# Performance work log

Hardware: AMD Instinct MI355X
Metric: run time of the kernel (lower is better)

The kernel has to match this reference:

```python
import jax, jax.numpy as jnp
import numpy as np

IN_FEATURES = 4096
OUT_FEATURES = 4096
IN_GROUP = 8
OUT_GROUP = 1
NUM_CODEBOOKS = 1
CODEBOOK_SIZE = 2 ** 16
NUM_OUT_GROUPS = OUT_FEATURES // OUT_GROUP   # 4096
NUM_IN_GROUPS = IN_FEATURES // IN_GROUP      # 512


def setup_inputs() -> dict:
    key = jax.random.key(0)
    k1, k2, k3, k4, k5 = jax.random.split(key, 5)
    input = jax.random.normal(k1, (4, 2048, IN_FEATURES), dtype=jnp.float32)
    codes = jax.random.randint(k2, (NUM_OUT_GROUPS, NUM_IN_GROUPS, NUM_CODEBOOKS), 0, CODEBOOK_SIZE, dtype=jnp.int32)
    codebooks = jax.random.normal(k3, (NUM_CODEBOOKS, CODEBOOK_SIZE, OUT_GROUP, IN_GROUP), dtype=jnp.float32)
    scales = jax.random.uniform(k4, (NUM_OUT_GROUPS, 1, 1, 1), dtype=jnp.float32)
    bias = jax.random.normal(k5, (OUT_FEATURES,), dtype=jnp.float32)
    return {"input": input, "codes": codes, "codebooks": codebooks, "scales": scales, "bias": bias}


def _dequantize_weight(codes, codebooks, scales):
    # codes: [nog, nig, nc] int; codebooks: [nc, K, og, ig]; scales: [nog, 1, 1, 1]
    nc = codebooks.shape[0]
    # gather per-codebook entries: [nog, nig, nc, og, ig]
    gathered = codebooks[jnp.arange(nc), codes]
    # sum over codebooks, apply per-out-group scale -> [nog, nig, og, ig]
    w = gathered.sum(axis=2) * scales
    nog, nig, og, ig = w.shape
    # [nog, og, nig, ig] -> [out_features, in_features]
    return w.transpose(0, 2, 1, 3).reshape(nog * og, nig * ig)


def reference(input, codes, codebooks, scales, bias):
    # Faithful AQLM dequant-GEMM: reconstruct W then input @ W^T + bias
    W = _dequantize_weight(codes, codebooks, scales)  # [out, in]
    out = jnp.einsum("bso,io->bsi", input, W.T.T) if False else input @ W.T
    if bias is not None:
        out = out + bias
    return out
```

## Files before the change

### kernel.cpp

```cpp
#include <hip/hip_runtime.h>
#include <hip/hip_bf16.h>
#include <stdint.h>

#define M_DIM 8192
#define N_DIM 4096
#define K_DIM 4096
#define NOG   4096
#define NIG   512

typedef __bf16 bf16;
typedef __attribute__((ext_vector_type(8))) __bf16 bf16x8;
typedef __attribute__((ext_vector_type(4))) float f32x4;

__device__ __forceinline__ void gload16(const void* g, void* lds) {
    __builtin_amdgcn_global_load_lds(
        (__attribute__((address_space(1))) void*)g,
        (__attribute__((address_space(3))) void*)lds,
        16 , 0 , 0 );
}

__global__ __launch_bounds__(256) void k_convert(const float* __restrict__ in,
                                                 bf16* __restrict__ out) {
    int i = blockIdx.x * blockDim.x + threadIdx.x;
    const float4* p = (const float4*)in + (size_t)i * 2;
    float4 a = p[0], b = p[1];
    bf16x8 o;
    o[0] = (bf16)a.x; o[1] = (bf16)a.y; o[2] = (bf16)a.z; o[3] = (bf16)a.w;
    o[4] = (bf16)b.x; o[5] = (bf16)b.y; o[6] = (bf16)b.z; o[7] = (bf16)b.w;
    ((bf16x8*)out)[i] = o;
}

__global__ __launch_bounds__(256) void k_dequant(const int* __restrict__ codes,
                                                 const float* __restrict__ cb,
                                                 const float* __restrict__ scales,
                                                 bf16* __restrict__ w) {
    int i = blockIdx.x * blockDim.x + threadIdx.x;
    int o = i >> 9;
    unsigned code = (unsigned)codes[i];
    float s = scales[o];
    const float4* e = (const float4*)(cb + (size_t)code * 8);
    float4 e0 = e[0], e1 = e[1];
    bf16x8 v;
    v[0] = (bf16)(e0.x * s); v[1] = (bf16)(e0.y * s);
    v[2] = (bf16)(e0.z * s); v[3] = (bf16)(e0.w * s);
    v[4] = (bf16)(e1.x * s); v[5] = (bf16)(e1.y * s);
    v[6] = (bf16)(e1.z * s); v[7] = (bf16)(e1.w * s);
    ((bf16x8*)w)[i] = v;
}

#define BM 128
#define BN 128
#define BK 32
#define KSTEPS (K_DIM / BK)

__global__ __launch_bounds__(256) void k_gemm_bt_bias(
    const bf16* __restrict__ A,
    const bf16* __restrict__ B,
    const float* __restrict__ bias,
    float* __restrict__ C)
{
    __shared__ __align__(16) bf16 As[BM * BK];
    __shared__ __align__(16) bf16 Bs[BN * BK];

    const int tid  = threadIdx.x;
    const int wave = tid >> 6;
    const int lane = tid & 63;
    const int quad = lane >> 4;
    const int l16  = lane & 15;

    const int bm0 = blockIdx.y * BM;
    const int bn0 = blockIdx.x * BN;

    const int wm = (wave >> 1) * 64;
    const int wn = (wave & 1) * 64;

    const int srow = lane >> 2;
    const int scol = (lane & 3) * 8;
    const bf16* Ag0 = A + (size_t)(bm0 + wave * 32 + srow) * K_DIM + scol;
    const bf16* Ag1 = Ag0 + (size_t)16 * K_DIM;
    const bf16* Bg0 = B + (size_t)(bn0 + wave * 32 + srow) * K_DIM + scol;
    const bf16* Bg1 = Bg0 + (size_t)16 * K_DIM;

    bf16* AsW = As + wave * 32 * BK;
    bf16* BsW = Bs + wave * 32 * BK;

    f32x4 acc[4][4] = {};

    for (int ks = 0; ks < KSTEPS; ++ks) {
        gload16(Ag0, AsW);
        gload16(Ag1, AsW + 16 * BK);
        gload16(Bg0, BsW);
        gload16(Bg1, BsW + 16 * BK);
        Ag0 += BK; Ag1 += BK; Bg0 += BK; Bg1 += BK;
        __syncthreads();

        bf16x8 af[4], bfr[4];
        #pragma unroll
        for (int t = 0; t < 4; ++t) {
            af[t]  = *(const bf16x8*)(As + (wm + t * 16 + l16) * BK + quad * 8);
            bfr[t] = *(const bf16x8*)(Bs + (wn + t * 16 + l16) * BK + quad * 8);
        }
        #pragma unroll
        for (int i = 0; i < 4; ++i)
            #pragma unroll
            for (int j = 0; j < 4; ++j)
                acc[i][j] = __builtin_amdgcn_mfma_f32_16x16x32_bf16(
                    af[i], bfr[j], acc[i][j], 0, 0, 0);

        __syncthreads();
    }

    #pragma unroll
    for (int j = 0; j < 4; ++j) {
        const int gn = bn0 + wn + j * 16 + l16;
        const float bz = bias[gn];
        #pragma unroll
        for (int i = 0; i < 4; ++i) {
            float* cp = C + (size_t)(bm0 + wm + i * 16 + quad * 4) * N_DIM + gn;
            #pragma unroll
            for (int r = 0; r < 4; ++r)
                cp[(size_t)r * N_DIM] = acc[i][j][r] + bz;
        }
    }
}

extern "C" void kernel_launch(void* const* d_in, const int* in_sizes, int n_in,
                              void* d_out, int out_size, void* d_ws, size_t ws_size,
                              hipStream_t stream) {
    const float* input     = (const float*)d_in[0];
    const int*   codes     = (const int*)d_in[1];
    const float* codebooks = (const float*)d_in[2];
    const float* scales    = (const float*)d_in[3];
    const float* bias      = (const float*)d_in[4];
    float* out = (float*)d_out;

    bf16* Abf = (bf16*)d_ws;
    bf16* Wbf = (bf16*)((char*)d_ws + (size_t)M_DIM * K_DIM * sizeof(bf16));

    (void)in_sizes; (void)n_in; (void)out_size; (void)ws_size;

    k_convert<<<(M_DIM * (size_t)K_DIM / 8) / 256, 256, 0, stream>>>(input, Abf);

    k_dequant<<<((size_t)NOG * NIG) / 256, 256, 0, stream>>>(codes, codebooks, scales, Wbf);

    dim3 grid(N_DIM / BN, M_DIM / BM);
    k_gemm_bt_bias<<<grid, 256, 0, stream>>>(Abf, Wbf, bias, out);
}
```

Measured before the change: 543.3 us.

## Enlarge GEMM M-tile to 256, XOR-swizzle LDS, coalesce convert kernel

```diff
diff --git a/kernel.cpp b/kernel.cpp
--- a/kernel.cpp
+++ b/kernel.cpp
@@ -10,6 +10,7 @@
 
 typedef __bf16 bf16;
 typedef __attribute__((ext_vector_type(8))) __bf16 bf16x8;
+typedef __attribute__((ext_vector_type(4))) __bf16 bf16x4;
 typedef __attribute__((ext_vector_type(4))) float f32x4;
 
 __device__ __forceinline__ void gload16(const void* g, void* lds) {
@@ -21,13 +22,14 @@
 
 __global__ __launch_bounds__(256) void k_convert(const float* __restrict__ in,
                                                  bf16* __restrict__ out) {
-    int i = blockIdx.x * blockDim.x + threadIdx.x;
-    const float4* p = (const float4*)in + (size_t)i * 2;
-    float4 a = p[0], b = p[1];
-    bf16x8 o;
-    o[0] = (bf16)a.x; o[1] = (bf16)a.y; o[2] = (bf16)a.z; o[3] = (bf16)a.w;
-    o[4] = (bf16)b.x; o[5] = (bf16)b.y; o[6] = (bf16)b.z; o[7] = (bf16)b.w;
-    ((bf16x8*)out)[i] = o;
+    int i0 = blockIdx.x * 512 + threadIdx.x;
+    const float4* p = (const float4*)in;
+    float4 a = p[i0], b = p[i0 + 256];
+    bf16x4 oa, ob;
+    oa[0] = (bf16)a.x; oa[1] = (bf16)a.y; oa[2] = (bf16)a.z; oa[3] = (bf16)a.w;
+    ob[0] = (bf16)b.x; ob[1] = (bf16)b.y; ob[2] = (bf16)b.z; ob[3] = (bf16)b.w;
+    ((bf16x4*)out)[i0]       = oa;
+    ((bf16x4*)out)[i0 + 256] = ob;
 }
 
 __global__ __launch_bounds__(256) void k_dequant(const int* __restrict__ codes,
@@ -48,12 +50,12 @@
     ((bf16x8*)w)[i] = v;
 }
 
-#define BM 128
+#define BM 256
 #define BN 128
 #define BK 32
 #define KSTEPS (K_DIM / BK)
 
-__global__ __launch_bounds__(256) void k_gemm_bt_bias(
+__global__ __launch_bounds__(256, 2) void k_gemm_bt_bias(
     const bf16* __restrict__ A,
     const bf16* __restrict__ B,
     const float* __restrict__ bias,
@@ -71,37 +73,44 @@
     const int bm0 = blockIdx.y * BM;
     const int bn0 = blockIdx.x * BN;
 
-    const int wm = (wave >> 1) * 64;
+    const int wm = (wave >> 1) * 128;
     const int wn = (wave & 1) * 64;
 
     const int srow = lane >> 2;
-    const int scol = (lane & 3) * 8;
-    const bf16* Ag0 = A + (size_t)(bm0 + wave * 32 + srow) * K_DIM + scol;
-    const bf16* Ag1 = Ag0 + (size_t)16 * K_DIM;
-    const bf16* Bg0 = B + (size_t)(bn0 + wave * 32 + srow) * K_DIM + scol;
-    const bf16* Bg1 = Bg0 + (size_t)16 * K_DIM;
+    const int sblk = (lane & 3) ^ (srow & 3);
+    const int scol = sblk * 8;
 
-    bf16* AsW = As + wave * 32 * BK;
+    const bf16* Ag = A + (size_t)(bm0 + wave * 64 + srow) * K_DIM + scol;
+    const bf16* Bg = B + (size_t)(bn0 + wave * 32 + srow) * K_DIM + scol;
+    bf16* AsW = As + wave * 64 * BK;
     bf16* BsW = Bs + wave * 32 * BK;
 
-    f32x4 acc[4][4] = {};
+    const int rblkA = (quad ^ (l16 & 3)) * 8;
+
+    f32x4 acc[8][4] = {};
+
+    const size_t rstep = (size_t)16 * K_DIM;
 
     for (int ks = 0; ks < KSTEPS; ++ks) {
-        gload16(Ag0, AsW);
-        gload16(Ag1, AsW + 16 * BK);
-        gload16(Bg0, BsW);
-        gload16(Bg1, BsW + 16 * BK);
-        Ag0 += BK; Ag1 += BK; Bg0 += BK; Bg1 += BK;
+        gload16(Ag,              AsW);
+        gload16(Ag + rstep,      AsW + 16 * BK);
+        gload16(Ag + 2 * rstep,  AsW + 32 * BK);
+        gload16(Ag + 3 * rstep,  AsW + 48 * BK);
+        gload16(Bg,              BsW);
+        gload16(Bg + rstep,      BsW + 16 * BK);
+        Ag += BK; Bg += BK;
         __syncthreads();
 
-        bf16x8 af[4], bfr[4];
+        bf16x8 af[8], bfr[4];
         #pragma unroll
-        for (int t = 0; t < 4; ++t) {
-            af[t]  = *(const bf16x8*)(As + (wm + t * 16 + l16) * BK + quad * 8);
-            bfr[t] = *(const bf16x8*)(Bs + (wn + t * 16 + l16) * BK + quad * 8);
-        }
+        for (int t = 0; t < 8; ++t)
+            af[t]  = *(const bf16x8*)(As + (wm + t * 16 + l16) * BK + rblkA);
         #pragma unroll
-        for (int i = 0; i < 4; ++i)
+        for (int t = 0; t < 4; ++t)
+            bfr[t] = *(const bf16x8*)(Bs + (wn + t * 16 + l16) * BK + rblkA);
+
+        #pragma unroll
+        for (int i = 0; i < 8; ++i)
             #pragma unroll
             for (int j = 0; j < 4; ++j)
                 acc[i][j] = __builtin_amdgcn_mfma_f32_16x16x32_bf16(
@@ -115,7 +124,7 @@
         const int gn = bn0 + wn + j * 16 + l16;
         const float bz = bias[gn];
         #pragma unroll
-        for (int i = 0; i < 4; ++i) {
+        for (int i = 0; i < 8; ++i) {
             float* cp = C + (size_t)(bm0 + wm + i * 16 + quad * 4) * N_DIM + gn;
             #pragma unroll
             for (int r = 0; r < 4; ++r)
@@ -139,7 +148,7 @@
 
     (void)in_sizes; (void)n_in; (void)out_size; (void)ws_size;
 
-    k_convert<<<(M_DIM * (size_t)K_DIM / 8) / 256, 256, 0, stream>>>(input, Abf);
+    k_convert<<<(M_DIM * (size_t)K_DIM / 4) / 512, 256, 0, stream>>>(input, Abf);
 
     k_dequant<<<((size_t)NOG * NIG) / 256, 256, 0, stream>>>(codes, codebooks, scales, Wbf);
 
```

Result: faster. 514.6 us (-5.3%).

## Enlarge GEMM tile to 256x128x64 with conflict-free fragment-ordered LDS layout

Applied to the files above, without the earlier changes.

```diff
diff --git a/kernel.cpp b/kernel.cpp
--- a/kernel.cpp
+++ b/kernel.cpp
@@ -48,12 +48,12 @@
     ((bf16x8*)w)[i] = v;
 }
 
-#define BM 128
+#define BM 256
 #define BN 128
-#define BK 32
+#define BK 64
 #define KSTEPS (K_DIM / BK)
 
-__global__ __launch_bounds__(256) void k_gemm_bt_bias(
+__global__ __launch_bounds__(256, 2) void k_gemm_bt_bias(
     const bf16* __restrict__ A,
     const bf16* __restrict__ B,
     const float* __restrict__ bias,
@@ -71,41 +71,62 @@
     const int bm0 = blockIdx.y * BM;
     const int bn0 = blockIdx.x * BN;
 
-    const int wm = (wave >> 1) * 64;
+    const int wm = (wave >> 1) * 128;
     const int wn = (wave & 1) * 64;
 
-    const int srow = lane >> 2;
-    const int scol = (lane & 3) * 8;
-    const bf16* Ag0 = A + (size_t)(bm0 + wave * 32 + srow) * K_DIM + scol;
-    const bf16* Ag1 = Ag0 + (size_t)16 * K_DIM;
-    const bf16* Bg0 = B + (size_t)(bn0 + wave * 32 + srow) * K_DIM + scol;
-    const bf16* Bg1 = Bg0 + (size_t)16 * K_DIM;
+    const int srow = lane & 15;
+    const int skb  = lane >> 4;
 
-    bf16* AsW = As + wave * 32 * BK;
-    bf16* BsW = Bs + wave * 32 * BK;
+    const bf16* Ag = A + (size_t)(bm0 + wave * 64 + srow) * K_DIM + skb * 8;
+    const bf16* Bg = B + (size_t)(bn0 + wave * 32 + srow) * K_DIM + skb * 8;
+    bf16* AsW = As + (size_t)(wave * 4 * 2) * 512;
+    bf16* BsW = Bs + (size_t)(wave * 2 * 2) * 512;
 
-    f32x4 acc[4][4] = {};
+    const size_t rstep = (size_t)16 * K_DIM;
+
+    const int gA0 = wm >> 4;
+    const int gB0 = wn >> 4;
+
+    f32x4 acc[8][4] = {};
 
     for (int ks = 0; ks < KSTEPS; ++ks) {
-        gload16(Ag0, AsW);
-        gload16(Ag1, AsW + 16 * BK);
-        gload16(Bg0, BsW);
-        gload16(Bg1, BsW + 16 * BK);
-        Ag0 += BK; Ag1 += BK; Bg0 += BK; Bg1 += BK;
+        #pragma unroll
+        for (int gi = 0; gi < 4; ++gi) {
+            gload16(Ag + gi * rstep,      AsW + (gi * 2 + 0) * 512);
+            gload16(Ag + gi * rstep + 32, AsW + (gi * 2 + 1) * 512);
+        }
+        #pragma unroll
+        for (int gi = 0; gi < 2; ++gi) {
+            gload16(Bg + gi * rstep,      BsW + (gi * 2 + 0) * 512);
+            gload16(Bg + gi * rstep + 32, BsW + (gi * 2 + 1) * 512);
+        }
+        Ag += BK; Bg += BK;
         __syncthreads();
 
-        bf16x8 af[4], bfr[4];
+        bf16x8 af0[8], af1[8], bf0[4], bf1[4];
+        #pragma unroll
+        for (int t = 0; t < 8; ++t) {
+            af0[t] = *(const bf16x8*)(As + ((size_t)((gA0 + t) * 2 + 0) * 64 + lane) * 8);
+            af1[t] = *(const bf16x8*)(As + ((size_t)((gA0 + t) * 2 + 1) * 64 + lane) * 8);
+        }
         #pragma unroll
         for (int t = 0; t < 4; ++t) {
-            af[t]  = *(const bf16x8*)(As + (wm + t * 16 + l16) * BK + quad * 8);
-            bfr[t] = *(const bf16x8*)(Bs + (wn + t * 16 + l16) * BK + quad * 8);
+            bf0[t] = *(const bf16x8*)(Bs + ((size_t)((gB0 + t) * 2 + 0) * 64 + lane) * 8);
+            bf1[t] = *(const bf16x8*)(Bs + ((size_t)((gB0 + t) * 2 + 1) * 64 + lane) * 8);
         }
+
         #pragma unroll
-        for (int i = 0; i < 4; ++i)
+        for (int i = 0; i < 8; ++i)
             #pragma unroll
             for (int j = 0; j < 4; ++j)
                 acc[i][j] = __builtin_amdgcn_mfma_f32_16x16x32_bf16(
-                    af[i], bfr[j], acc[i][j], 0, 0, 0);
+                    af0[i], bf0[j], acc[i][j], 0, 0, 0);
+        #pragma unroll
+        for (int i = 0; i < 8; ++i)
+            #pragma unroll
+            for (int j = 0; j < 4; ++j)
+                acc[i][j] = __builtin_amdgcn_mfma_f32_16x16x32_bf16(
+                    af1[i], bf1[j], acc[i][j], 0, 0, 0);
 
         __syncthreads();
     }
@@ -115,7 +136,7 @@
         const int gn = bn0 + wn + j * 16 + l16;
         const float bz = bias[gn];
         #pragma unroll
-        for (int i = 0; i < 4; ++i) {
+        for (int i = 0; i < 8; ++i) {
             float* cp = C + (size_t)(bm0 + wm + i * 16 + quad * 4) * N_DIM + gn;
             #pragma unroll
             for (int r = 0; r < 4; ++r)
```

Result: slower. 599.8 us (+10.4%).
